# Kernel tuning notes

Measured on AMD Instinct MI355X. Metric: run time of the kernel, lower is better.

## Reference

```python
import jax, jax.numpy as jnp
import numpy as np

B, N, D, LAT, EC = 1024, 256, 64, 128, 32


def setup_inputs() -> dict:
    key = jax.random.key(0)
    ks = jax.random.split(key, 8)
    s = lambda d: 1.0 / np.sqrt(d)
    return {
        "local_data": jax.random.normal(ks[0], (B, D), jnp.float32),
        "neighbor_data": jax.random.normal(ks[1], (B, N, D), jnp.float32),
        "Wc": jax.random.normal(ks[2], (D, EC), jnp.float32) * s(D),
        "bc": jnp.zeros((EC,), jnp.float32),
        "Wf": jax.random.normal(ks[3], (D, LAT), jnp.float32) * s(D),
        "bf": jnp.zeros((LAT,), jnp.float32),
        "Wa": jax.random.normal(ks[4], (3 * EC, LAT), jnp.float32) * s(3 * EC),
        "ba": jnp.zeros((LAT,), jnp.float32),
        "Wl": jax.random.normal(ks[5], (LAT, LAT), jnp.float32) * s(LAT),
        "bl": jnp.zeros((LAT,), jnp.float32),
    }


def reference(local_data, neighbor_data, Wc, bc, Wf, bf, Wa, ba, Wl, bl):
    # per-neighbor feature encoder: [B,N,LAT]
    enc_feature = jax.nn.relu(jnp.einsum("bnd,dk->bnk", neighbor_data, Wf) + bf)
    # per-neighbor communication encoder: [B,N,EC]
    enc_comm = jax.nn.relu(jnp.einsum("bnd,dk->bnk", neighbor_data, Wc) + bc)
    # self communication embedding: [B,EC]
    enc_comm_self = jax.nn.relu(local_data @ Wc + bc)
    # broadcast self and neighbor-mean to [B,N,EC]
    self_rep = jnp.broadcast_to(enc_comm_self[:, None, :], enc_comm.shape)
    mean_rep = jnp.broadcast_to(enc_comm.mean(axis=1, keepdims=True), enc_comm.shape)
    cat = jnp.concatenate([self_rep, enc_comm, mean_rep], axis=-1)  # [B,N,3*EC]
    # attention: linear then softmax over neighbor axis (dim=-2)
    att = jax.nn.softmax(jnp.einsum("bnc,ck->bnk", cat, Wa) + ba, axis=1)  # [B,N,LAT]
    # attention-weighted sum over neighbors: [B,LAT]
    aggregated = jnp.einsum("bnk,bnk->bk", att, enc_feature)
    # later layer
    return jax.nn.relu(aggregated @ Wl + bl)
```

## Files before the change

### kernel.cpp

```cpp
#include <hip/hip_runtime.h>

#define NB    256
#define DIN   64
#define LATD  128
#define ECD   32

typedef __attribute__((ext_vector_type(8))) __bf16 bf16x8;
typedef __attribute__((ext_vector_type(4))) float f32x4;

#define XS_STRIDE 72
#define EC_STRIDE 40
#define WA_STRIDE 40

#define WS_WC 0
#define WS_WF (32 * 72)
#define WS_WA (32 * 72 + 128 * 72)

#define MFMA(a, b, c) __builtin_amdgcn_mfma_f32_16x16x32_bf16((a), (b), (c), 0, 0, 0)

__device__ __forceinline__ unsigned short f2bf(float f) {
    unsigned u = __builtin_bit_cast(unsigned, f);
    u += 0x7fffu + ((u >> 16) & 1u);
    return (unsigned short)(u >> 16);
}

__device__ __forceinline__ bf16x8 pack8(float4 a, float4 b) {
    union { unsigned short u[8]; bf16x8 v; } r;
    r.u[0] = f2bf(a.x); r.u[1] = f2bf(a.y); r.u[2] = f2bf(a.z); r.u[3] = f2bf(a.w);
    r.u[4] = f2bf(b.x); r.u[5] = f2bf(b.y); r.u[6] = f2bf(b.z); r.u[7] = f2bf(b.w);
    return r.v;
}

__global__ __launch_bounds__(256) void prep_kernel(
    const float* __restrict__ Wc, const float* __restrict__ Wf,
    const float* __restrict__ Wa, unsigned short* __restrict__ ws)
{
    int t = blockIdx.x * blockDim.x + threadIdx.x;
    int stride = gridDim.x * blockDim.x;
    for (int i = t; i < 32 * 64; i += stride) {
        int n = i >> 6, k = i & 63;
        ws[WS_WC + n * XS_STRIDE + k] = f2bf(Wc[k * ECD + n]);
    }
    for (int i = t; i < 128 * 64; i += stride) {
        int n = i >> 6, k = i & 63;
        ws[WS_WF + n * XS_STRIDE + k] = f2bf(Wf[k * LATD + n]);
    }
    for (int i = t; i < 128 * 32; i += stride) {
        int n = i >> 5, k = i & 31;
        ws[WS_WA + n * WA_STRIDE + k] = f2bf(Wa[(ECD + k) * LATD + n]);
    }
}

__global__ __launch_bounds__(256, 4) void arm_main(
    const float* __restrict__ xg,
    const float* __restrict__ bcv,
    const float* __restrict__ bfv,
    const float* __restrict__ wl,
    const float* __restrict__ blv,
    const unsigned short* __restrict__ ws,
    float* __restrict__ out)
{
    __shared__ unsigned short ecs[NB * EC_STRIDE];
    __shared__ float aggnum[4][LATD];
    __shared__ float aggden[4][LATD];
    __shared__ float aggfull[LATD];
    __shared__ float wlpart[2][LATD];

    const int b    = blockIdx.x;
    const int tid  = threadIdx.x;
    const int lane = tid & 63;
    const int w    = tid >> 6;
    const int l15  = lane & 15;
    const int q    = lane >> 4;

    const float* xb = xg + (size_t)b * NB * DIN;
    float4 st[4][4];
    #pragma unroll
    for (int t = 0; t < 4; ++t) {
        const float* p = xb + (w * 64 + t * 16 + l15) * DIN + q * 8;
        st[t][0] = *reinterpret_cast<const float4*>(p);
        st[t][1] = *reinterpret_cast<const float4*>(p + 4);
        st[t][2] = *reinterpret_cast<const float4*>(p + 32);
        st[t][3] = *reinterpret_cast<const float4*>(p + 36);
    }
    bf16x8 xfrag[4][2];
    #pragma unroll
    for (int t = 0; t < 4; ++t) {
        xfrag[t][0] = pack8(st[t][0], st[t][1]);
        xfrag[t][1] = pack8(st[t][2], st[t][3]);
    }

    {
        bf16x8 wfrag[2][2];
        #pragma unroll
        for (int ks = 0; ks < 2; ++ks)
            #pragma unroll
            for (int nb = 0; nb < 2; ++nb)
                wfrag[ks][nb] = *reinterpret_cast<const bf16x8*>(
                    &ws[WS_WC + (nb * 16 + l15) * XS_STRIDE + ks * 32 + q * 8]);

        float bc0 = bcv[l15], bc1 = bcv[16 + l15];
        #pragma unroll
        for (int t = 0; t < 4; ++t) {
            int rowA = w * 64 + t * 16;
            f32x4 a0 = {0.f, 0.f, 0.f, 0.f}, a1 = {0.f, 0.f, 0.f, 0.f};
            #pragma unroll
            for (int ks = 0; ks < 2; ++ks) {
                a0 = MFMA(xfrag[t][ks], wfrag[ks][0], a0);
                a1 = MFMA(xfrag[t][ks], wfrag[ks][1], a1);
            }
            #pragma unroll
            for (int r = 0; r < 4; ++r) {
                int row = rowA + q * 4 + r;
                ecs[row * EC_STRIDE + l15]      = f2bf(fmaxf(a0[r] + bc0, 0.f));
                ecs[row * EC_STRIDE + 16 + l15] = f2bf(fmaxf(a1[r] + bc1, 0.f));
            }
        }
    }

    bf16x8 ecfrag[4];
    #pragma unroll
    for (int t = 0; t < 4; ++t)
        ecfrag[t] = *reinterpret_cast<const bf16x8*>(
            &ecs[(w * 64 + t * 16 + l15) * EC_STRIDE + q * 8]);

    for (int g = 0; g < 8; ++g) {
        bf16x8 wf0 = *reinterpret_cast<const bf16x8*>(
            &ws[WS_WF + (g * 16 + l15) * XS_STRIDE + q * 8]);
        bf16x8 wf1 = *reinterpret_cast<const bf16x8*>(
            &ws[WS_WF + (g * 16 + l15) * XS_STRIDE + 32 + q * 8]);
        bf16x8 wag = *reinterpret_cast<const bf16x8*>(
            &ws[WS_WA + (g * 16 + l15) * WA_STRIDE + q * 8]);

        f32x4 ef[4], lg[4];
        #pragma unroll
        for (int t = 0; t < 4; ++t) {
            f32x4 z = {0.f, 0.f, 0.f, 0.f};
            z = MFMA(xfrag[t][0], wf0, z);
            ef[t] = MFMA(xfrag[t][1], wf1, z);
            f32x4 z2 = {0.f, 0.f, 0.f, 0.f};
            lg[t] = MFMA(ecfrag[t], wag, z2);
        }
        float bfl = bfv[g * 16 + l15];
        float num = 0.f, den = 0.f;
        #pragma unroll
        for (int t = 0; t < 4; ++t)
            #pragma unroll
            for (int r = 0; r < 4; ++r) {
                float e = fmaxf(ef[t][r] + bfl, 0.f);
                float p = exp2f(lg[t][r] * 1.44269504f);
                num += p * e;
                den += p;
            }
        num += __shfl_xor(num, 16, 64); num += __shfl_xor(num, 32, 64);
        den += __shfl_xor(den, 16, 64); den += __shfl_xor(den, 32, 64);
        if (lane < 16) {
            aggnum[w][g * 16 + lane] = num;
            aggden[w][g * 16 + lane] = den;
        }
    }
    __syncthreads();

    if (tid < 128) {
        float num = aggnum[0][tid] + aggnum[1][tid] + aggnum[2][tid] + aggnum[3][tid];
        float den = aggden[0][tid] + aggden[1][tid] + aggden[2][tid] + aggden[3][tid];
        aggfull[tid] = num / den;
    }
    __syncthreads();

    {
        int c = tid & 127, h = tid >> 7;
        float acc = 0.f;
        #pragma unroll 16
        for (int k = h * 64; k < h * 64 + 64; ++k)
            acc += aggfull[k] * wl[k * LATD + c];
        wlpart[h][c] = acc;
    }
    __syncthreads();
    if (tid < 128)
        out[(size_t)b * LATD + tid] =
            fmaxf(wlpart[0][tid] + wlpart[1][tid] + blv[tid], 0.f);
}

extern "C" void kernel_launch(void* const* d_in, const int* in_sizes, int n_in,
                              void* d_out, int out_size, void* d_ws, size_t ws_size,
                              hipStream_t stream)
{
    const float* xg  = (const float*)d_in[1];
    const float* wc  = (const float*)d_in[2];
    const float* bc_ = (const float*)d_in[3];
    const float* wf  = (const float*)d_in[4];
    const float* bf_ = (const float*)d_in[5];
    const float* wa  = (const float*)d_in[6];
    const float* wl  = (const float*)d_in[8];
    const float* bl_ = (const float*)d_in[9];
    unsigned short* wsp = (unsigned short*)d_ws;
    float* out = (float*)d_out;

    prep_kernel<<<8, 256, 0, stream>>>(wc, wf, wa, wsp);
    arm_main<<<1024, 256, 0, stream>>>(xg, bc_, bf_, wl, bl_, wsp, out);
}
```

Baseline: 129.1 us.

## Split each batch row across 8 waves and use packed bf16 conversion

Doubles the block size from 256 to 512 threads, so each wave handles 32 neighbor rows instead of 64. Per-wave partial sums and the final Wl matvec are spread over more partitions. The scalar bf16 rounding helper is replaced by the packed v_cvt_pk_bf16_f32 instruction for input and comm-encoder conversion. Communication fragments are now loaded from LDS inside the loop, and the g loop is unrolled by 2. The aim is lower register pressure, more waves in flight to hide global-load latency, and fewer conversion instructions, at the cost of more LDS reduction work and larger blocks.

```diff
diff --git a/kernel.cpp b/kernel.cpp
--- a/kernel.cpp
+++ b/kernel.cpp
@@ -24,10 +24,18 @@
     return (unsigned short)(u >> 16);
 }
 
+__device__ __forceinline__ unsigned cvt2(float lo, float hi) {
+    unsigned r;
+    asm("v_cvt_pk_bf16_f32 %0, %1, %2" : "=v"(r) : "v"(lo), "v"(hi));
+    return r;
+}
+
 __device__ __forceinline__ bf16x8 pack8(float4 a, float4 b) {
-    union { unsigned short u[8]; bf16x8 v; } r;
-    r.u[0] = f2bf(a.x); r.u[1] = f2bf(a.y); r.u[2] = f2bf(a.z); r.u[3] = f2bf(a.w);
-    r.u[4] = f2bf(b.x); r.u[5] = f2bf(b.y); r.u[6] = f2bf(b.z); r.u[7] = f2bf(b.w);
+    union { unsigned u[4]; bf16x8 v; } r;
+    r.u[0] = cvt2(a.x, a.y);
+    r.u[1] = cvt2(a.z, a.w);
+    r.u[2] = cvt2(b.x, b.y);
+    r.u[3] = cvt2(b.z, b.w);
     return r.v;
 }
 
@@ -51,7 +59,7 @@
     }
 }
 
-__global__ __launch_bounds__(256, 4) void arm_main(
+__global__ __launch_bounds__(512, 8) void arm_main(
     const float* __restrict__ xg,
     const float* __restrict__ bcv,
     const float* __restrict__ bfv,
@@ -61,10 +69,10 @@
     float* __restrict__ out)
 {
     __shared__ unsigned short ecs[NB * EC_STRIDE];
-    __shared__ float aggnum[4][LATD];
-    __shared__ float aggden[4][LATD];
+    __shared__ float aggnum[8][LATD];
+    __shared__ float aggden[8][LATD];
     __shared__ float aggfull[LATD];
-    __shared__ float wlpart[2][LATD];
+    __shared__ float wlpart[4][LATD];
 
     const int b    = blockIdx.x;
     const int tid  = threadIdx.x;
@@ -74,20 +82,16 @@
     const int q    = lane >> 4;
 
     const float* xb = xg + (size_t)b * NB * DIN;
-    float4 st[4][4];
+    bf16x8 xfrag[2][2];
     #pragma unroll
-    for (int t = 0; t < 4; ++t) {
-        const float* p = xb + (w * 64 + t * 16 + l15) * DIN + q * 8;
-        st[t][0] = *reinterpret_cast<const float4*>(p);
-        st[t][1] = *reinterpret_cast<const float4*>(p + 4);
-        st[t][2] = *reinterpret_cast<const float4*>(p + 32);
-        st[t][3] = *reinterpret_cast<const float4*>(p + 36);
-    }
-    bf16x8 xfrag[4][2];
-    #pragma unroll
-    for (int t = 0; t < 4; ++t) {
-        xfrag[t][0] = pack8(st[t][0], st[t][1]);
-        xfrag[t][1] = pack8(st[t][2], st[t][3]);
+    for (int t = 0; t < 2; ++t) {
+        const float* p = xb + (w * 32 + t * 16 + l15) * DIN + q * 8;
+        float4 s0 = *reinterpret_cast<const float4*>(p);
+        float4 s1 = *reinterpret_cast<const float4*>(p + 4);
+        float4 s2 = *reinterpret_cast<const float4*>(p + 32);
+        float4 s3 = *reinterpret_cast<const float4*>(p + 36);
+        xfrag[t][0] = pack8(s0, s1);
+        xfrag[t][1] = pack8(s2, s3);
     }
 
     {
@@ -101,8 +105,8 @@
 
         float bc0 = bcv[l15], bc1 = bcv[16 + l15];
         #pragma unroll
-        for (int t = 0; t < 4; ++t) {
-            int rowA = w * 64 + t * 16;
+        for (int t = 0; t < 2; ++t) {
+            int rowA = w * 32 + t * 16;
             f32x4 a0 = {0.f, 0.f, 0.f, 0.f}, a1 = {0.f, 0.f, 0.f, 0.f};
             #pragma unroll
             for (int ks = 0; ks < 2; ++ks) {
@@ -112,18 +116,18 @@
             #pragma unroll
             for (int r = 0; r < 4; ++r) {
                 int row = rowA + q * 4 + r;
-                ecs[row * EC_STRIDE + l15]      = f2bf(fmaxf(a0[r] + bc0, 0.f));
-                ecs[row * EC_STRIDE + 16 + l15] = f2bf(fmaxf(a1[r] + bc1, 0.f));
+                unsigned pk = cvt2(fmaxf(a0[r] + bc0, 0.f),
+                                   fmaxf(a1[r] + bc1, 0.f));
+                ecs[row * EC_STRIDE + l15]      = (unsigned short)pk;
+                ecs[row * EC_STRIDE + 16 + l15] = (unsigned short)(pk >> 16);
             }
         }
     }
 
-    bf16x8 ecfrag[4];
-    #pragma unroll
-    for (int t = 0; t < 4; ++t)
-        ecfrag[t] = *reinterpret_cast<const bf16x8*>(
-            &ecs[(w * 64 + t * 16 + l15) * EC_STRIDE + q * 8]);
-
+    const unsigned short* ecp0 = &ecs[(w * 32 + l15) * EC_STRIDE + q * 8];
+    const unsigned short* ecp1 = &ecs[(w * 32 + 16 + l15) * EC_STRIDE + q * 8];
+
+    #pragma unroll 2
     for (int g = 0; g < 8; ++g) {
         bf16x8 wf0 = *reinterpret_cast<const bf16x8*>(
             &ws[WS_WF + (g * 16 + l15) * XS_STRIDE + q * 8]);
@@ -131,27 +135,25 @@
             &ws[WS_WF + (g * 16 + l15) * XS_STRIDE + 32 + q * 8]);
         bf16x8 wag = *reinterpret_cast<const bf16x8*>(
             &ws[WS_WA + (g * 16 + l15) * WA_STRIDE + q * 8]);
-
-        f32x4 ef[4], lg[4];
-        #pragma unroll
-        for (int t = 0; t < 4; ++t) {
+        float bfl = bfv[g * 16 + l15];
+
+        float num = 0.f, den = 0.f;
+        #pragma unroll
+        for (int t = 0; t < 2; ++t) {
+            bf16x8 ecf = *reinterpret_cast<const bf16x8*>(t ? ecp1 : ecp0);
             f32x4 z = {0.f, 0.f, 0.f, 0.f};
             z = MFMA(xfrag[t][0], wf0, z);
-            ef[t] = MFMA(xfrag[t][1], wf1, z);
+            f32x4 ef = MFMA(xfrag[t][1], wf1, z);
             f32x4 z2 = {0.f, 0.f, 0.f, 0.f};
-            lg[t] = MFMA(ecfrag[t], wag, z2);
-        }
-        float bfl = bfv[g * 16 + l15];
-        float num = 0.f, den = 0.f;
-        #pragma unroll
-        for (int t = 0; t < 4; ++t)
+            f32x4 lg = MFMA(ecf, wag, z2);
             #pragma unroll
             for (int r = 0; r < 4; ++r) {
-                float e = fmaxf(ef[t][r] + bfl, 0.f);
-                float p = exp2f(lg[t][r] * 1.44269504f);
-                num += p * e;
+                float e = fmaxf(ef[r] + bfl, 0.f);
+                float p = exp2f(lg[r] * 1.44269504f);
+                num = fmaf(p, e, num);
                 den += p;
             }
+        }
         num += __shfl_xor(num, 16, 64); num += __shfl_xor(num, 32, 64);
         den += __shfl_xor(den, 16, 64); den += __shfl_xor(den, 32, 64);
         if (lane < 16) {
@@ -162,8 +164,12 @@
     __syncthreads();
 
     if (tid < 128) {
-        float num = aggnum[0][tid] + aggnum[1][tid] + aggnum[2][tid] + aggnum[3][tid];
-        float den = aggden[0][tid] + aggden[1][tid] + aggden[2][tid] + aggden[3][tid];
+        float num = 0.f, den = 0.f;
+        #pragma unroll
+        for (int i = 0; i < 8; ++i) {
+            num += aggnum[i][tid];
+            den += aggden[i][tid];
+        }
         aggfull[tid] = num / den;
     }
     __syncthreads();
@@ -171,15 +177,16 @@
     {
         int c = tid & 127, h = tid >> 7;
         float acc = 0.f;
-        #pragma unroll 16
-        for (int k = h * 64; k < h * 64 + 64; ++k)
+        #pragma unroll 8
+        for (int k = h * 32; k < h * 32 + 32; ++k)
             acc += aggfull[k] * wl[k * LATD + c];
         wlpart[h][c] = acc;
     }
     __syncthreads();
     if (tid < 128)
         out[(size_t)b * LATD + tid] =
-            fmaxf(wlpart[0][tid] + wlpart[1][tid] + blv[tid], 0.f);
+            fmaxf(wlpart[0][tid] + wlpart[1][tid] + wlpart[2][tid] +
+                      wlpart[3][tid] + blv[tid], 0.f);
 }
 
 extern "C" void kernel_launch(void* const* d_in, const int* in_sizes, int n_in,
@@ -198,5 +205,5 @@
     float* out = (float*)d_out;
 
     prep_kernel<<<8, 256, 0, stream>>>(wc, wf, wa, wsp);
-    arm_main<<<1024, 256, 0, stream>>>(xg, bc_, bf_, wl, bl_, wsp, out);
-}
+    arm_main<<<1024, 512, 0, stream>>>(xg, bc_, bf_, wl, bl_, wsp, out);
+}
```

Result: slower. 138.1 us (+7.0%).
